# Kernel tuning notes

Measured on AMD Instinct MI355X. Metric: run time of the kernel, lower is better.

## Reference

```python
import jax, jax.numpy as jnp
import numpy as np

B, H_IN, H_OUT, SEQ_LEN = 256, 512, 512, 512


def setup_inputs() -> dict:
    key = jax.random.key(0)
    k1, k2, k3, k4, k5 = jax.random.split(key, 5)
    s = 1.0 / np.sqrt(H_OUT)  # torch GRU init scale
    return {
        "x": jax.random.normal(k1, (B, H_IN), dtype=jnp.float32),
        "W_ih": jax.random.uniform(k2, (3 * H_OUT, H_IN), jnp.float32, -s, s),
        "W_hh": jax.random.uniform(k3, (3 * H_OUT, H_OUT), jnp.float32, -s, s),
        "b_ih": jax.random.uniform(k4, (3 * H_OUT,), jnp.float32, -s, s),
        "b_hh": jax.random.uniform(k5, (3 * H_OUT,), jnp.float32, -s, s),
        "seq_len": SEQ_LEN,
    }


def reference(x, W_ih, W_hh, b_ih, b_hh, seq_len):
    # bridge: ReLU, then the same vector is fed at every timestep, so the
    # input-to-hidden projection is computed ONCE and reused across the scan.
    xr = jax.nn.relu(x)                       # [B, H_in]
    gi = xr @ W_ih.T + b_ih                   # [B, 3*H_out], constant over time
    Hh = W_hh.shape[1]
    gi_r, gi_z, gi_n = gi[:, :Hh], gi[:, Hh:2 * Hh], gi[:, 2 * Hh:]

    h0 = jnp.zeros((x.shape[0], Hh), dtype=x.dtype)

    def step(h, _):
        gh = h @ W_hh.T + b_hh                # [B, 3*H_out]
        gh_r, gh_z, gh_n = gh[:, :Hh], gh[:, Hh:2 * Hh], gh[:, 2 * Hh:]
        r = jax.nn.sigmoid(gi_r + gh_r)
        z = jax.nn.sigmoid(gi_z + gh_z)
        n = jnp.tanh(gi_n + r * gh_n)
        h_new = (1.0 - z) * n + z * h
        return h_new, h_new

    _, hs = jax.lax.scan(step, h0, None, length=seq_len)  # [S, B, H_out]
    return jnp.transpose(hs, (1, 0, 2))                   # [B, S, H_out]
```

## Files before the change

### kernel.cpp

```cpp
#include <hip/hip_runtime.h>


typedef __attribute__((ext_vector_type(8))) short short8;
typedef __attribute__((ext_vector_type(4))) float f32x4;
typedef __attribute__((ext_vector_type(2))) float f32x2;
typedef __attribute__((ext_vector_type(4))) unsigned int u32x4;
typedef unsigned short ushort_t;
typedef unsigned int uint_t;
typedef unsigned long long u64_t;

#define NG 16
#define NM 16
#define NB 16
#define NJ 32
#define TPB 384
#define SPIN_MAX (1u << 16)
#define ABORT_IDX 8192
#define GBUF_BASE 16384
#define GRP_U32 8192
#define BUF_U32 131072

__device__ __forceinline__ uint_t ald32(const uint_t* p) {
  return __hip_atomic_load(p, __ATOMIC_RELAXED, __HIP_MEMORY_SCOPE_AGENT);
}
__device__ __forceinline__ u64_t ald64(const u64_t* p) {
  return __hip_atomic_load(p, __ATOMIC_RELAXED, __HIP_MEMORY_SCOPE_AGENT);
}
__device__ __forceinline__ ushort_t bf16_rne(float f) {
  uint_t u = __float_as_uint(f);
  return (ushort_t)((u + 0x7fffu + ((u >> 16) & 1u)) >> 16);
}
__device__ __forceinline__ float bf16f(ushort_t h) {
  return __uint_as_float(((uint_t)h) << 16);
}
__device__ __forceinline__ int gRow(int rs, int m) {
  int base = m * NJ;
  if (rs < 32) return base + rs;
  if (rs < 64) return 512 + base + (rs - 32);
  return 1024 + base + (rs - 64);
}

template <bool LO>
__device__ __forceinline__ void loadW(short8* dst, const float* __restrict__ W,
                                      int tile, int m, int lane) {
  int rs = tile * 16 + (lane & 15);
  const float* p = W + (size_t)gRow(rs, m) * 512 + ((lane >> 4) << 3);
#pragma unroll
  for (int c = 0; c < 16; ++c) {
    const float* pc = p + c * 32;
    short8 o;
#pragma unroll
    for (int i = 0; i < 8; ++i) {
      float v = pc[i];
      ushort_t hi = bf16_rne(v);
      o[i] = LO ? (short)bf16_rne(v - bf16f(hi)) : (short)hi;
    }
    dst[c] = o;
  }
}

__global__ __launch_bounds__(TPB, 1) void gru_kernel(
    const float* __restrict__ x, const float* __restrict__ Wih,
    const float* __restrict__ Whh, const float* __restrict__ bih,
    const float* __restrict__ bhh, float* __restrict__ out,
    uint_t* __restrict__ wsp, int NT) {
  __shared__ __align__(16) uint_t s_pb[16 * 512];
  __shared__ float s_gi[96 * 17];
  __shared__ float s_gh[96 * 17];
  __shared__ float s_hloc[NB * NJ];
  __shared__ float s_bhh[NJ];
  __shared__ int s_stop;

  const int tid = threadIdx.x;
  const int lane = tid & 63;
  const int w = tid >> 6;
  const int bid = blockIdx.x;
  const int g = bid & 15;
  const int m = bid >> 4;
  if (NT <= 0) return;

  uint_t* flags = wsp;
  uint_t* gbuf = wsp + GBUF_BASE;

  for (int i = tid; i < 1024; i += TPB) {
    int b = i >> 6, k0 = (i & 63) << 3;
    const float* px = x + (size_t)(g * NB + b) * 512 + k0;
    u32x4 vh, vl;
#pragma unroll
    for (int jj = 0; jj < 4; ++jj) {
      float f0 = px[2 * jj], f1 = px[2 * jj + 1];
      f0 = f0 > 0.f ? f0 : 0.f;
      f1 = f1 > 0.f ? f1 : 0.f;
      ushort_t h0 = bf16_rne(f0), h1 = bf16_rne(f1);
      vh[jj] = (uint_t)h0 | ((uint_t)h1 << 16);
      vl[jj] = (uint_t)bf16_rne(f0 - bf16f(h0)) |
               ((uint_t)bf16_rne(f1 - bf16f(h1)) << 16);
    }
    int c = k0 >> 5, kk = k0 & 31;
    int base = c * 2048 + (((b << 6) + (kk << 1)) ^ ((b & 7) << 4));
    *(u32x4*)((char*)s_pb + base) = vh;
    *(u32x4*)((char*)s_pb + base + 1024) = vl;
  }
  if (tid < NJ) s_bhh[tid] = bhh[1024 + m * NJ + tid];
  if (tid == 0) s_stop = 0;
  __syncthreads();

  short8 wA[16], wB[16];
  const f32x4 vzero = {0.f, 0.f, 0.f, 0.f};
  const int bcol = lane & 15;
  const int roff = ((bcol << 6) + ((lane >> 4) << 4)) ^ ((bcol & 7) << 4);
  const char* pb = (const char*)s_pb;

  f32x4 acc0 = vzero, acc1 = vzero;
  if (w < 3) {
    loadW<false>(wA, Wih, 2 * w, m, lane);
    loadW<false>(wB, Wih, 2 * w + 1, m, lane);
    {
      f32x4 a0h = vzero, a0l = vzero, a1h = vzero, a1l = vzero;
#pragma unroll
      for (int c = 0; c < 16; ++c) {
        short8 bh = *(const short8*)(pb + c * 2048 + roff);
        short8 bl = *(const short8*)(pb + c * 2048 + 1024 + roff);
        a0h = __builtin_amdgcn_mfma_f32_16x16x32_bf16(wA[c], bh, a0h, 0, 0, 0);
        a1h = __builtin_amdgcn_mfma_f32_16x16x32_bf16(wB[c], bh, a1h, 0, 0, 0);
        a0l = __builtin_amdgcn_mfma_f32_16x16x32_bf16(wA[c], bl, a0l, 0, 0, 0);
        a1l = __builtin_amdgcn_mfma_f32_16x16x32_bf16(wB[c], bl, a1l, 0, 0, 0);
      }
      acc0 = a0h + a0l;
      acc1 = a1h + a1l;
    }
    loadW<true>(wA, Wih, 2 * w, m, lane);
    loadW<true>(wB, Wih, 2 * w + 1, m, lane);
#pragma unroll
    for (int c = 0; c < 16; ++c) {
      short8 bh = *(const short8*)(pb + c * 2048 + roff);
      acc0 = __builtin_amdgcn_mfma_f32_16x16x32_bf16(wA[c], bh, acc0, 0, 0, 0);
      acc1 = __builtin_amdgcn_mfma_f32_16x16x32_bf16(wB[c], bh, acc1, 0, 0, 0);
    }
  }
  __syncthreads();
  if (w < 3) {
    int drow = (lane >> 4) << 2;
#pragma unroll
    for (int q = 0; q < 4; ++q) {
      int rs0 = 2 * w * 16 + drow + q, rs1 = rs0 + 16;
      int g0 = gRow(rs0, m), g1 = gRow(rs1, m);
      s_gi[rs0 * 17 + bcol] = acc0[q] + bih[g0] + (rs0 < 64 ? bhh[g0] : 0.f);
      s_gi[rs1 * 17 + bcol] = acc1[q] + bih[g1] + (rs1 < 64 ? bhh[g1] : 0.f);
    }
    loadW<false>(wA, Whh, 2 * w, m, lane);
    loadW<false>(wB, Whh, 2 * w + 1, m, lane);
  }
  for (int i = tid; i < 8192; i += TPB) s_pb[i] = 0u;
  for (int i = tid; i < NB * NJ; i += TPB) s_hloc[i] = 0.f;
  __syncthreads();

  const size_t outRow = (size_t)NT * 512;
  float* outBase = out + (size_t)(g * NB) * outRow + m * NJ;

  for (int t = 0; t < NT; ++t) {
    if (w < 3) {
      f32x4 a0h = vzero, a0l = vzero, a1h = vzero, a1l = vzero;
#pragma unroll
      for (int p = 0; p < 16; ++p) {
        short8 bh = *(const short8*)(pb + p * 2048 + roff);
        short8 bl = *(const short8*)(pb + p * 2048 + 1024 + roff);
        a0h = __builtin_amdgcn_mfma_f32_16x16x32_bf16(wA[p], bh, a0h, 0, 0, 0);
        a1h = __builtin_amdgcn_mfma_f32_16x16x32_bf16(wB[p], bh, a1h, 0, 0, 0);
        a0l = __builtin_amdgcn_mfma_f32_16x16x32_bf16(wA[p], bl, a0l, 0, 0, 0);
        a1l = __builtin_amdgcn_mfma_f32_16x16x32_bf16(wB[p], bl, a1l, 0, 0, 0);
      }
      f32x4 r0 = a0h + a0l, r1 = a1h + a1l;
      int drow = (lane >> 4) << 2;
#pragma unroll
      for (int q = 0; q < 4; ++q) {
        s_gh[(2 * w * 16 + drow + q) * 17 + bcol] = r0[q];
        s_gh[((2 * w + 1) * 16 + drow + q) * 17 + bcol] = r1[q];
      }
    }
    __syncthreads();

    const int gt = tid - 64;
    float hn0 = 0.f, hn1 = 0.f;
    uint_t* eb =
        gbuf + (size_t)((t & 1) ^ 1) * BUF_U32 + g * GRP_U32 + m * 512;
    if ((unsigned)gt < 256u) {
      int b = gt >> 4, j0 = (gt & 15) << 1;
      {
        int j = j0;
        float pr = s_gi[j * 17 + b] + s_gh[j * 17 + b];
        float pz = s_gi[(32 + j) * 17 + b] + s_gh[(32 + j) * 17 + b];
        float r = 1.f / (1.f + __expf(-pr));
        float z = 1.f / (1.f + __expf(-pz));
        float pn =
            s_gi[(64 + j) * 17 + b] + r * (s_gh[(64 + j) * 17 + b] + s_bhh[j]);
        float n = 1.f - 2.f / (1.f + __expf(2.f * pn));
        hn0 = n + z * (s_hloc[b * 32 + j] - n);
        s_hloc[b * 32 + j] = hn0;
      }
      {
        int j = j0 + 1;
        float pr = s_gi[j * 17 + b] + s_gh[j * 17 + b];
        float pz = s_gi[(32 + j) * 17 + b] + s_gh[(32 + j) * 17 + b];
        float r = 1.f / (1.f + __expf(-pr));
        float z = 1.f / (1.f + __expf(-pz));
        float pn =
            s_gi[(64 + j) * 17 + b] + r * (s_gh[(64 + j) * 17 + b] + s_bhh[j]);
        float n = 1.f - 2.f / (1.f + __expf(2.f * pn));
        hn1 = n + z * (s_hloc[b * 32 + j] - n);
        s_hloc[b * 32 + j] = hn1;
      }
      ushort_t hA = bf16_rne(hn0), hB = bf16_rne(hn1);
      uint_t phi = (uint_t)hA | ((uint_t)hB << 16);
      uint_t plo = (uint_t)bf16_rne(hn0 - bf16f(hA)) |
                   ((uint_t)bf16_rne(hn1 - bf16f(hB)) << 16);
      __hip_atomic_store(eb + gt, phi, __ATOMIC_RELAXED,
                         __HIP_MEMORY_SCOPE_AGENT);
      __hip_atomic_store(eb + 256 + gt, plo, __ATOMIC_RELAXED,
                         __HIP_MEMORY_SCOPE_AGENT);
    }
    __syncthreads();

    if (tid == 256)
      __hip_atomic_store(&flags[((g << 4) + m) << 5], (uint_t)(t + 1),
                         __ATOMIC_RELAXED, __HIP_MEMORY_SCOPE_AGENT);
    if ((unsigned)gt < 256u) {
      int b = gt >> 4, j0 = (gt & 15) << 1;
      f32x2 ov = {hn0, hn1};
      __builtin_nontemporal_store(
          ov, (f32x2*)(outBase + (size_t)b * outRow + (size_t)t * 512 + j0));
    }
    if (w == 5 && t + 1 < NT) {
      const uint_t tgt = (uint_t)(t + 1);
      uint_t* fp = flags + (((g << 4) + (lane & 15)) << 5);
      uint_t sp = 0;
      for (;;) {
        uint_t v = 0xffffffffu;
        if (lane < 16) v = ald32(fp);
        if (__all((int)(v >= tgt))) break;
        ++sp;
        uint_t ab = 0;
        if ((sp & 127u) == 0u) {
          ab = ald32(&flags[ABORT_IDX]);
          if (sp > SPIN_MAX) {
            __hip_atomic_store(&flags[ABORT_IDX], 1u, __ATOMIC_RELAXED,
                               __HIP_MEMORY_SCOPE_AGENT);
            ab = 1;
          }
        }
        if (__any((int)(ab != 0))) {
          if (lane == 0) s_stop = 1;
          break;
        }
        __builtin_amdgcn_s_sleep(1);
      }
    }
    __syncthreads();
    if (s_stop) break;

    if (t + 1 < NT) {
      const u64_t* srcq =
          (const u64_t*)(gbuf + (size_t)((t + 1) & 1) * BUF_U32 + g * GRP_U32);
#define LDI(k) ald64(srcq + tid + (k) * TPB)
      u64_t q0 = LDI(0), q1 = LDI(1), q2 = LDI(2), q3 = LDI(3), q4 = LDI(4);
      u64_t q5 = LDI(5), q6 = LDI(6), q7 = LDI(7), q8 = LDI(8), q9 = LDI(9);
      u64_t q10 = (tid < 256) ? LDI(10) : 0ull;
#undef LDI
#define STI(k, qq)                                                             \
  {                                                                            \
    uint_t qb = (uint_t)(tid + (k) * TPB) << 3;                                \
    *(u64_t*)((char*)s_pb + (qb ^ (((qb >> 6) & 7u) << 4))) = (qq);            \
  }
      STI(0, q0) STI(1, q1) STI(2, q2) STI(3, q3) STI(4, q4)
      STI(5, q5) STI(6, q6) STI(7, q7) STI(8, q8) STI(9, q9)
      if (tid < 256) STI(10, q10)
#undef STI
      __syncthreads();
    }
  }
}

extern "C" void kernel_launch(void* const* d_in, const int* in_sizes, int n_in,
                              void* d_out, int out_size, void* d_ws,
                              size_t ws_size, hipStream_t stream) {
  const float* x = (const float*)d_in[0];
  const float* Wih = (const float*)d_in[1];
  const float* Whh = (const float*)d_in[2];
  const float* bih = (const float*)d_in[3];
  const float* bhh = (const float*)d_in[4];
  float* out = (float*)d_out;
  int NT = out_size / (256 * 512);
  uint_t* wsp = (uint_t*)d_ws;
  (void)hipMemsetAsync(d_ws, 0, 65536, stream);
  hipLaunchKernelGGL(gru_kernel, dim3(NG * NM), dim3(TPB), 0, stream, x, Wih,
                     Whh, bih, bhh, out, wsp, NT);
}
```

Before: 1.294 ms.

## Exchange hidden state as single bf16 and split flag polling across waves

The recurrent hidden state is now exchanged between blocks as bf16-high only, dropping the low-residual half. This halves the global exchange traffic and the recurrent MFMA count per step, with two interleaved accumulators kept for ILP. The gate computation moves to 128 threads handling 4 outputs each, writing packed 64-bit stores and 16-byte output stores. Flag polling and refill are split so each of 4 waves waits only on its 4 producer blocks and copies its own slice, which drops one block-wide barrier per step. The cost is reduced precision in the recurrence, since the h residual term is removed.

```diff
diff --git a/kernel.cpp b/kernel.cpp
--- a/kernel.cpp
+++ b/kernel.cpp
@@ -3,7 +3,6 @@
 
 typedef __attribute__((ext_vector_type(8))) short short8;
 typedef __attribute__((ext_vector_type(4))) float f32x4;
-typedef __attribute__((ext_vector_type(2))) float f32x2;
 typedef __attribute__((ext_vector_type(4))) unsigned int u32x4;
 typedef unsigned short ushort_t;
 typedef unsigned int uint_t;
@@ -17,15 +16,12 @@
 #define SPIN_MAX (1u << 16)
 #define ABORT_IDX 8192
 #define GBUF_BASE 16384
-#define GRP_U32 8192
-#define BUF_U32 131072
-
-__device__ __forceinline__ uint_t ald32(const uint_t* p) {
-  return __hip_atomic_load(p, __ATOMIC_RELAXED, __HIP_MEMORY_SCOPE_AGENT);
-}
-__device__ __forceinline__ u64_t ald64(const u64_t* p) {
-  return __hip_atomic_load(p, __ATOMIC_RELAXED, __HIP_MEMORY_SCOPE_AGENT);
-}
+#define GRP_U32 4096
+#define BUF_U32 65536
+
+#define ALD(P) __hip_atomic_load((P), __ATOMIC_RELAXED, __HIP_MEMORY_SCOPE_AGENT)
+#define AST(P, V) __hip_atomic_store((P), (V), __ATOMIC_RELAXED, __HIP_MEMORY_SCOPE_AGENT)
+
 __device__ __forceinline__ ushort_t bf16_rne(float f) {
   uint_t u = __float_as_uint(f);
   return (ushort_t)((u + 0x7fffu + ((u >> 16) & 1u)) >> 16);
@@ -64,7 +60,8 @@
     const float* __restrict__ Whh, const float* __restrict__ bih,
     const float* __restrict__ bhh, float* __restrict__ out,
     uint_t* __restrict__ wsp, int NT) {
-  __shared__ __align__(16) uint_t s_pb[16 * 512];
+  __shared__ __align__(16) uint_t s_pb[4096];
+  __shared__ __align__(16) uint_t s_xlo[4096];
   __shared__ float s_gi[96 * 17];
   __shared__ float s_gh[96 * 17];
   __shared__ float s_hloc[NB * NJ];
@@ -77,6 +74,7 @@
   const int bid = blockIdx.x;
   const int g = bid & 15;
   const int m = bid >> 4;
+  const int me = (g << 4) + m;
   if (NT <= 0) return;
 
   uint_t* flags = wsp;
@@ -97,9 +95,9 @@
                ((uint_t)bf16_rne(f1 - bf16f(h1)) << 16);
     }
     int c = k0 >> 5, kk = k0 & 31;
-    int base = c * 2048 + (((b << 6) + (kk << 1)) ^ ((b & 7) << 4));
+    int base = c * 1024 + ((((b << 6) + (kk << 1))) ^ ((b & 7) << 4));
     *(u32x4*)((char*)s_pb + base) = vh;
-    *(u32x4*)((char*)s_pb + base + 1024) = vl;
+    *(u32x4*)((char*)s_xlo + base) = vl;
   }
   if (tid < NJ) s_bhh[tid] = bhh[1024 + m * NJ + tid];
   if (tid == 0) s_stop = 0;
@@ -110,6 +108,7 @@
   const int bcol = lane & 15;
   const int roff = ((bcol << 6) + ((lane >> 4) << 4)) ^ ((bcol & 7) << 4);
   const char* pb = (const char*)s_pb;
+  const char* pxl = (const char*)s_xlo;
 
   f32x4 acc0 = vzero, acc1 = vzero;
   if (w < 3) {
@@ -119,8 +118,8 @@
       f32x4 a0h = vzero, a0l = vzero, a1h = vzero, a1l = vzero;
 #pragma unroll
       for (int c = 0; c < 16; ++c) {
-        short8 bh = *(const short8*)(pb + c * 2048 + roff);
-        short8 bl = *(const short8*)(pb + c * 2048 + 1024 + roff);
+        short8 bh = *(const short8*)(pb + c * 1024 + roff);
+        short8 bl = *(const short8*)(pxl + c * 1024 + roff);
         a0h = __builtin_amdgcn_mfma_f32_16x16x32_bf16(wA[c], bh, a0h, 0, 0, 0);
         a1h = __builtin_amdgcn_mfma_f32_16x16x32_bf16(wB[c], bh, a1h, 0, 0, 0);
         a0l = __builtin_amdgcn_mfma_f32_16x16x32_bf16(wA[c], bl, a0l, 0, 0, 0);
@@ -133,7 +132,7 @@
     loadW<true>(wB, Wih, 2 * w + 1, m, lane);
 #pragma unroll
     for (int c = 0; c < 16; ++c) {
-      short8 bh = *(const short8*)(pb + c * 2048 + roff);
+      short8 bh = *(const short8*)(pb + c * 1024 + roff);
       acc0 = __builtin_amdgcn_mfma_f32_16x16x32_bf16(wA[c], bh, acc0, 0, 0, 0);
       acc1 = __builtin_amdgcn_mfma_f32_16x16x32_bf16(wB[c], bh, acc1, 0, 0, 0);
     }
@@ -151,7 +150,7 @@
     loadW<false>(wA, Whh, 2 * w, m, lane);
     loadW<false>(wB, Whh, 2 * w + 1, m, lane);
   }
-  for (int i = tid; i < 8192; i += TPB) s_pb[i] = 0u;
+  for (int i = tid; i < 4096; i += TPB) s_pb[i] = 0u;
   for (int i = tid; i < NB * NJ; i += TPB) s_hloc[i] = 0.f;
   __syncthreads();
 
@@ -160,17 +159,17 @@
 
   for (int t = 0; t < NT; ++t) {
     if (w < 3) {
-      f32x4 a0h = vzero, a0l = vzero, a1h = vzero, a1l = vzero;
-#pragma unroll
-      for (int p = 0; p < 16; ++p) {
-        short8 bh = *(const short8*)(pb + p * 2048 + roff);
-        short8 bl = *(const short8*)(pb + p * 2048 + 1024 + roff);
-        a0h = __builtin_amdgcn_mfma_f32_16x16x32_bf16(wA[p], bh, a0h, 0, 0, 0);
-        a1h = __builtin_amdgcn_mfma_f32_16x16x32_bf16(wB[p], bh, a1h, 0, 0, 0);
-        a0l = __builtin_amdgcn_mfma_f32_16x16x32_bf16(wA[p], bl, a0l, 0, 0, 0);
-        a1l = __builtin_amdgcn_mfma_f32_16x16x32_bf16(wB[p], bl, a1l, 0, 0, 0);
-      }
-      f32x4 r0 = a0h + a0l, r1 = a1h + a1l;
+      f32x4 aE0 = vzero, aO0 = vzero, aE1 = vzero, aO1 = vzero;
+#pragma unroll
+      for (int p = 0; p < 16; p += 2) {
+        short8 b0 = *(const short8*)(pb + p * 1024 + roff);
+        short8 b1 = *(const short8*)(pb + (p + 1) * 1024 + roff);
+        aE0 = __builtin_amdgcn_mfma_f32_16x16x32_bf16(wA[p], b0, aE0, 0, 0, 0);
+        aE1 = __builtin_amdgcn_mfma_f32_16x16x32_bf16(wB[p], b0, aE1, 0, 0, 0);
+        aO0 = __builtin_amdgcn_mfma_f32_16x16x32_bf16(wA[p + 1], b1, aO0, 0, 0, 0);
+        aO1 = __builtin_amdgcn_mfma_f32_16x16x32_bf16(wB[p + 1], b1, aO1, 0, 0, 0);
+      }
+      f32x4 r0 = aE0 + aO0, r1 = aE1 + aO1;
       int drow = (lane >> 4) << 2;
 #pragma unroll
       for (int q = 0; q < 4; ++q) {
@@ -180,14 +179,16 @@
     }
     __syncthreads();
 
-    const int gt = tid - 64;
-    float hn0 = 0.f, hn1 = 0.f;
-    uint_t* eb =
-        gbuf + (size_t)((t & 1) ^ 1) * BUF_U32 + g * GRP_U32 + m * 512;
-    if ((unsigned)gt < 256u) {
-      int b = gt >> 4, j0 = (gt & 15) << 1;
-      {
-        int j = j0;
+    const int et = tid - 256;
+    float hn[4];
+    int eb_ = 0, ej0 = 0;
+    if (et >= 0) {
+      int b = et >> 3, j0 = (et & 7) << 2;
+      eb_ = b;
+      ej0 = j0;
+#pragma unroll
+      for (int e = 0; e < 4; ++e) {
+        int j = j0 + e;
         float pr = s_gi[j * 17 + b] + s_gh[j * 17 + b];
         float pz = s_gi[(32 + j) * 17 + b] + s_gh[(32 + j) * 17 + b];
         float r = 1.f / (1.f + __expf(-pr));
@@ -195,88 +196,77 @@
         float pn =
             s_gi[(64 + j) * 17 + b] + r * (s_gh[(64 + j) * 17 + b] + s_bhh[j]);
         float n = 1.f - 2.f / (1.f + __expf(2.f * pn));
-        hn0 = n + z * (s_hloc[b * 32 + j] - n);
-        s_hloc[b * 32 + j] = hn0;
-      }
+        hn[e] = n + z * (s_hloc[b * 32 + j] - n);
+        s_hloc[b * 32 + j] = hn[e];
+      }
+      uint_t w0 = (uint_t)bf16_rne(hn[0]) | ((uint_t)bf16_rne(hn[1]) << 16);
+      uint_t w1 = (uint_t)bf16_rne(hn[2]) | ((uint_t)bf16_rne(hn[3]) << 16);
+      u64_t pq = (u64_t)w0 | ((u64_t)w1 << 32);
+      u64_t* eb64 =
+          (u64_t*)(gbuf + (size_t)((t & 1) ^ 1) * BUF_U32 + g * GRP_U32);
+      __hip_atomic_store(eb64 + (m << 7) + (eb_ << 3) + (et & 7), pq,
+                         __ATOMIC_RELAXED, __HIP_MEMORY_SCOPE_AGENT);
+    }
+    __syncthreads();
+
+    if (tid == 256)
+      AST(&flags[me << 5], (uint_t)(t + 1));
+    if (et >= 0) {
+      f32x4 ov = {hn[0], hn[1], hn[2], hn[3]};
+      __builtin_nontemporal_store(
+          ov,
+          (f32x4*)(outBase + (size_t)eb_ * outRow + (size_t)t * 512 + ej0));
+    }
+    if (w < 4 && t + 1 < NT) {
+      const uint_t tgt = (uint_t)(t + 1);
+      int ok = 1;
       {
-        int j = j0 + 1;
-        float pr = s_gi[j * 17 + b] + s_gh[j * 17 + b];
-        float pz = s_gi[(32 + j) * 17 + b] + s_gh[(32 + j) * 17 + b];
-        float r = 1.f / (1.f + __expf(-pr));
-        float z = 1.f / (1.f + __expf(-pz));
-        float pn =
-            s_gi[(64 + j) * 17 + b] + r * (s_gh[(64 + j) * 17 + b] + s_bhh[j]);
-        float n = 1.f - 2.f / (1.f + __expf(2.f * pn));
-        hn1 = n + z * (s_hloc[b * 32 + j] - n);
-        s_hloc[b * 32 + j] = hn1;
-      }
-      ushort_t hA = bf16_rne(hn0), hB = bf16_rne(hn1);
-      uint_t phi = (uint_t)hA | ((uint_t)hB << 16);
-      uint_t plo = (uint_t)bf16_rne(hn0 - bf16f(hA)) |
-                   ((uint_t)bf16_rne(hn1 - bf16f(hB)) << 16);
-      __hip_atomic_store(eb + gt, phi, __ATOMIC_RELAXED,
-                         __HIP_MEMORY_SCOPE_AGENT);
-      __hip_atomic_store(eb + 256 + gt, plo, __ATOMIC_RELAXED,
-                         __HIP_MEMORY_SCOPE_AGENT);
-    }
-    __syncthreads();
-
-    if (tid == 256)
-      __hip_atomic_store(&flags[((g << 4) + m) << 5], (uint_t)(t + 1),
-                         __ATOMIC_RELAXED, __HIP_MEMORY_SCOPE_AGENT);
-    if ((unsigned)gt < 256u) {
-      int b = gt >> 4, j0 = (gt & 15) << 1;
-      f32x2 ov = {hn0, hn1};
-      __builtin_nontemporal_store(
-          ov, (f32x2*)(outBase + (size_t)b * outRow + (size_t)t * 512 + j0));
-    }
-    if (w == 5 && t + 1 < NT) {
-      const uint_t tgt = (uint_t)(t + 1);
-      uint_t* fp = flags + (((g << 4) + (lane & 15)) << 5);
-      uint_t sp = 0;
-      for (;;) {
-        uint_t v = 0xffffffffu;
-        if (lane < 16) v = ald32(fp);
-        if (__all((int)(v >= tgt))) break;
-        ++sp;
-        uint_t ab = 0;
-        if ((sp & 127u) == 0u) {
-          ab = ald32(&flags[ABORT_IDX]);
-          if (sp > SPIN_MAX) {
-            __hip_atomic_store(&flags[ABORT_IDX], 1u, __ATOMIC_RELAXED,
-                               __HIP_MEMORY_SCOPE_AGENT);
-            ab = 1;
+        uint_t sp = 0;
+        uint_t* fp = flags + (((g << 4) + (w << 2) + (lane & 3)) << 5);
+        for (;;) {
+          uint_t v = tgt;
+          if (lane < 4) v = ALD(fp);
+          if (__all((int)(v >= tgt))) break;
+          ++sp;
+          uint_t ab = 0;
+          if ((sp & 127u) == 0u) {
+            ab = ALD(&flags[ABORT_IDX]);
+            if (sp > SPIN_MAX) {
+              AST(&flags[ABORT_IDX], 1u);
+              ab = 1;
+            }
           }
+          if (__any((int)(ab != 0))) {
+            if (lane == 0) s_stop = 1;
+            ok = 0;
+            break;
+          }
+          __builtin_amdgcn_s_sleep(1);
         }
-        if (__any((int)(ab != 0))) {
-          if (lane == 0) s_stop = 1;
-          break;
-        }
-        __builtin_amdgcn_s_sleep(1);
-      }
-    }
-    __syncthreads();
-    if (s_stop) break;
-
-    if (t + 1 < NT) {
-      const u64_t* srcq =
-          (const u64_t*)(gbuf + (size_t)((t + 1) & 1) * BUF_U32 + g * GRP_U32);
-#define LDI(k) ald64(srcq + tid + (k) * TPB)
-      u64_t q0 = LDI(0), q1 = LDI(1), q2 = LDI(2), q3 = LDI(3), q4 = LDI(4);
-      u64_t q5 = LDI(5), q6 = LDI(6), q7 = LDI(7), q8 = LDI(8), q9 = LDI(9);
-      u64_t q10 = (tid < 256) ? LDI(10) : 0ull;
+      }
+      if (ok) {
+        const u64_t* srcq =
+            (const u64_t*)(gbuf + (size_t)((t + 1) & 1) * BUF_U32 +
+                           g * GRP_U32) +
+            (w << 9);
+#define LDI(k)                                                                 \
+  __hip_atomic_load(srcq + lane + ((k) << 6), __ATOMIC_RELAXED,                \
+                    __HIP_MEMORY_SCOPE_AGENT)
+        u64_t q0 = LDI(0), q1 = LDI(1), q2 = LDI(2), q3 = LDI(3);
+        u64_t q4 = LDI(4), q5 = LDI(5), q6 = LDI(6), q7 = LDI(7);
 #undef LDI
 #define STI(k, qq)                                                             \
   {                                                                            \
-    uint_t qb = (uint_t)(tid + (k) * TPB) << 3;                                \
+    uint_t qb = (uint_t)(((w << 9) + lane + ((k) << 6)) << 3);                 \
     *(u64_t*)((char*)s_pb + (qb ^ (((qb >> 6) & 7u) << 4))) = (qq);            \
   }
-      STI(0, q0) STI(1, q1) STI(2, q2) STI(3, q3) STI(4, q4)
-      STI(5, q5) STI(6, q6) STI(7, q7) STI(8, q8) STI(9, q9)
-      if (tid < 256) STI(10, q10)
+        STI(0, q0) STI(1, q1) STI(2, q2) STI(3, q3)
+        STI(4, q4) STI(5, q5) STI(6, q6) STI(7, q7)
 #undef STI
-      __syncthreads();
-    }
+      }
+    }
+    __syncthreads();
+    if (s_stop) break;
   }
 }
 
```

After: 1.162 ms (median of 2 runs). 1.11x faster.
